# Optimization experiments

Measured on AMD Instinct MI355X. Metric: run time of the kernel, lower is better.

## Reference

```python
import jax, jax.numpy as jnp
import numpy as np

N = 100000
E = 1600000
CIN = 32
COUT = 32
K = 5
EPS = 1e-15      # PyG GMMConv EPS in sigma^2 denominator
BN_EPS = 1e-5    # torch BatchNorm1d default eps


def gmm_conv(x, edge_index, edge_attr, g, mu, sigma, root, bias):
    """PyG GMMConv (MoNet), aggr='mean', root_weight=True, bias=True."""
    src, dst = edge_index[0], edge_index[1]
    n = x.shape[0]
    k = mu.shape[0]
    cout = root.shape[1]
    xg = (x @ g).reshape(n, k, cout)                # [N, K, out]
    xj = xg[src]                                    # gather: [E, K, out]
    d = edge_attr[:, None, :] - mu[None, :, :]      # [E, K, 3]
    w = jnp.exp(-0.5 * jnp.sum(d * d / (EPS + sigma[None] ** 2), axis=-1))  # [E, K]
    msg = jnp.einsum('eko,ek->eo', xj, w)           # [E, out]
    agg = jax.ops.segment_sum(msg, dst, num_segments=n)
    cnt = jax.ops.segment_sum(jnp.ones((msg.shape[0],), x.dtype), dst, num_segments=n)
    agg = agg / jnp.clip(cnt, 1.0)[:, None]         # mean aggregation
    return agg + x @ root + bias


def batch_norm(x, gamma, beta):
    # training-mode BatchNorm1d: biased batch statistics over node dim
    m = x.mean(0)
    v = x.var(0)
    return (x - m) * jax.lax.rsqrt(v + BN_EPS) * gamma + beta


def setup_inputs() -> dict:
    key = jax.random.key(0)
    ks = jax.random.split(key, 12)
    p = lambda k, s, sc=0.1: jax.random.normal(k, s, jnp.float32) * sc
    return {
        'x': jax.random.normal(ks[0], (N, CIN), jnp.float32),
        'edge_index': jax.random.randint(ks[1], (2, E), 0, N, jnp.int32),
        'edge_attr': jax.random.uniform(ks[2], (E, 3), jnp.float32),
        # left conv1: in -> out, K=5
        'g1': p(ks[3], (CIN, K * COUT)), 'mu1': p(ks[4], (K, 3), 1.0), 'sigma1': jnp.ones((K, 3), jnp.float32),
        'root1': p(ks[5], (CIN, COUT)), 'b1': jnp.zeros((COUT,), jnp.float32),
        'gam1': jnp.ones((COUT,), jnp.float32), 'bet1': jnp.zeros((COUT,), jnp.float32),
        # left conv2: out -> out, K=5
        'g2': p(ks[6], (COUT, K * COUT)), 'mu2': p(ks[7], (K, 3), 1.0), 'sigma2': jnp.ones((K, 3), jnp.float32),
        'root2': p(ks[8], (COUT, COUT)), 'b2': jnp.zeros((COUT,), jnp.float32),
        'gam2': jnp.ones((COUT,), jnp.float32), 'bet2': jnp.zeros((COUT,), jnp.float32),
        # shortcut conv: in -> out, K=1
        'gs': p(ks[9], (CIN, 1 * COUT)), 'mus': p(ks[10], (1, 3), 1.0), 'sigmas': jnp.ones((1, 3), jnp.float32),
        'roots': p(ks[11], (CIN, COUT)), 'bs': jnp.zeros((COUT,), jnp.float32),
        'gams': jnp.ones((COUT,), jnp.float32), 'bets': jnp.zeros((COUT,), jnp.float32),
    }


def reference(x, edge_index, edge_attr,
              g1, mu1, sigma1, root1, b1, gam1, bet1,
              g2, mu2, sigma2, root2, b2, gam2, bet2,
              gs, mus, sigmas, roots, bs, gams, bets):
    h = jax.nn.elu(batch_norm(gmm_conv(x, edge_index, edge_attr, g1, mu1, sigma1, root1, b1), gam1, bet1))
    h = batch_norm(gmm_conv(h, edge_index, edge_attr, g2, mu2, sigma2, root2, b2), gam2, bet2)
    s = batch_norm(gmm_conv(x, edge_index, edge_attr, gs, mus, sigmas, roots, bs), gams, bets)
    return jax.nn.elu(h + s)
```

## Files before the change

### kernel.cpp

```cpp
#include <hip/hip_runtime.h>
#include <hip/hip_bf16.h>
#include <math.h>


#define ELU(v) ((v) > 0.f ? (v) : (__expf(v) - 1.f))

using short8  = __attribute__((ext_vector_type(8))) short;
using floatx4 = __attribute__((ext_vector_type(4))) float;

__device__ inline ushort f2bf(float f) {
    __hip_bfloat16 h = __float2bfloat16(f);
    return *reinterpret_cast<ushort*>(&h);
}
__device__ inline float bflo(unsigned u) { return __uint_as_float(u << 16); }
__device__ inline float bfhi(unsigned u) { return __uint_as_float(u & 0xffff0000u); }
__device__ inline unsigned pack_bf2(float lo, float hi) {
    return ((unsigned)f2bf(hi) << 16) | (unsigned)f2bf(lo);
}

__global__ __launch_bounds__(256) void prep_xb(
    const float* __restrict__ x, unsigned* __restrict__ XB, int N)
{
    const int idx = blockIdx.x * blockDim.x + threadIdx.x;
    if (idx >= N * 16) return;
    const float2 p = ((const float2*)x)[idx];
    XB[idx] = pack_bf2(p.x, p.y);
}

__global__ __launch_bounds__(256) void prep_hxb(
    const float* __restrict__ out1, const float* __restrict__ coef,
    unsigned* __restrict__ XB, int N)
{
    const int idx = blockIdx.x * blockDim.x + threadIdx.x;
    if (idx >= N * 16) return;
    const int l = idx & 15;
    const float2 p = ((const float2*)out1)[idx];
    const int c0 = 2 * l, c1 = 2 * l + 1;
    float v0 = p.x * coef[c0] + coef[32 + c0];
    float v1 = p.y * coef[c1] + coef[32 + c1];
    v0 = ELU(v0); v1 = ELU(v1);
    XB[idx] = pack_bf2(v0, v1);
}

#define CH 4096
__global__ __launch_bounds__(256) void binfill_k(
    const int* __restrict__ ei, const float* __restrict__ attr,
    int* __restrict__ gcur, unsigned long long* __restrict__ pay0,
    int E, int NB, int CAPc)
{
    __shared__ unsigned long long srec[CH];
    __shared__ unsigned char sbin[CH];
    __shared__ int cnt[256], offs[256], wcur[256], gbase[256], sc[256];

    const int t = threadIdx.x;
    const int e0 = blockIdx.x * CH;
    const int nrec = min(CH, E - e0);

    cnt[t] = 0;
    __syncthreads();

    unsigned long long rec[16];
    int bin[16];
#pragma unroll
    for (int r = 0; r < 16; ++r) {
        const int e = e0 + r * 256 + t;
        bin[r] = -1;
        if (e < E) {
            const int s = ei[e], d = ei[E + e];
            const float a0 = attr[(size_t)e * 3 + 0];
            const float a1 = attr[(size_t)e * 3 + 1];
            const float a2 = attr[(size_t)e * 3 + 2];
            const unsigned q0 = (unsigned)min(max((int)(a0 * 4096.f), 0), 4095);
            const unsigned q1 = (unsigned)min(max((int)(a1 * 4096.f), 0), 4095);
            const unsigned q2 = (unsigned)min(max((int)(a2 * 4096.f), 0), 4095);
            rec[r] = (unsigned long long)(unsigned)s
                   | ((unsigned long long)(d & 511) << 17)
                   | ((unsigned long long)q0 << 26)
                   | ((unsigned long long)q1 << 38)
                   | ((unsigned long long)q2 << 50);
            bin[r] = d >> 9;
            atomicAdd(&cnt[bin[r]], 1);
        }
    }
    __syncthreads();

    const int v = cnt[t];
    sc[t] = v;
    __syncthreads();
    for (int o = 1; o < 256; o <<= 1) {
        const int xx = (t >= o) ? sc[t - o] : 0;
        __syncthreads();
        sc[t] += xx;
        __syncthreads();
    }
    offs[t] = sc[t] - v;
    wcur[t] = sc[t] - v;
    __syncthreads();

#pragma unroll
    for (int r = 0; r < 16; ++r) {
        if (bin[r] >= 0) {
            const int pos = atomicAdd(&wcur[bin[r]], 1);
            srec[pos] = rec[r];
            sbin[pos] = (unsigned char)bin[r];
        }
    }
    __syncthreads();

    if (t < NB && cnt[t] > 0) gbase[t] = atomicAdd(&gcur[t], cnt[t]);
    __syncthreads();

    for (int i = t; i < nrec; i += 256) {
        const int b = sbin[i];
        const int idx = gbase[b] + (i - offs[b]);
        if (idx < CAPc)
            pay0[(size_t)b * CAPc + idx] = srec[i];
    }
}

__global__ __launch_bounds__(256) void scatter2_k(
    const unsigned long long* __restrict__ pay0, const int* __restrict__ gcur,
    int* __restrict__ row_ptr, unsigned long long* __restrict__ pay,
    int N, int CAPc, int NB)
{
    const int b = blockIdx.x;
    const int t = threadIdx.x;
    const int d0 = b << 9;
    const int nd = min(512, N - d0);

    __shared__ int cnt[512];
    __shared__ int offs[512];
    __shared__ int sscan[256];
    __shared__ int ssum[256];

    ssum[t] = (t < b && t < NB) ? gcur[t] : 0;
    for (int i = t; i < 512; i += 256) cnt[i] = 0;
    __syncthreads();
    for (int o = 128; o > 0; o >>= 1) {
        if (t < o) ssum[t] += ssum[t + o];
        __syncthreads();
    }
    const int base = ssum[0];

    const int total = min(gcur[b], CAPc);
    const unsigned long long* src = pay0 + (size_t)b * CAPc;

    for (int i = t; i < total; i += 256) {
        const int dlo = (int)((src[i] >> 17) & 511);
        atomicAdd(&cnt[dlo], 1);
    }
    __syncthreads();

    const int c0 = cnt[2 * t], c1 = cnt[2 * t + 1];
    const int pairsum = c0 + c1;
    sscan[t] = pairsum;
    __syncthreads();
    for (int o = 1; o < 256; o <<= 1) {
        const int xx = (t >= o) ? sscan[t - o] : 0;
        __syncthreads();
        sscan[t] += xx;
        __syncthreads();
    }
    const int excl = sscan[t] - pairsum;
    offs[2 * t] = excl;
    offs[2 * t + 1] = excl + c0;
    __syncthreads();
    const int btotal = sscan[255];

    for (int i = t; i < nd; i += 256) row_ptr[d0 + i] = base + offs[i];
    if (b == NB - 1 && t == 0) row_ptr[N] = base + btotal;

    for (int i = t; i < 512; i += 256) cnt[i] = offs[i];
    __syncthreads();

    for (int i = t; i < total; i += 256) {
        const unsigned long long rec = src[i];
        const int dlo = (int)((rec >> 17) & 511);
        const int p = atomicAdd(&cnt[dlo], 1);
        pay[base + p] = rec;
    }
}

template <bool HAS_S>
__global__ __launch_bounds__(256) void gt_k(
    const unsigned* __restrict__ XB,
    const unsigned long long* __restrict__ payload,
    const int* __restrict__ row_ptr,
    const float* __restrict__ mu_m, const float* __restrict__ sg_m,
    const float* __restrict__ mu_s, const float* __restrict__ sg_s,
    const float* __restrict__ g,
    const float* __restrict__ rootm,
    const float* __restrict__ bm,
    const float* __restrict__ gss,
    const float* __restrict__ rootss,
    const float* __restrict__ bss,
    float* __restrict__ out_m, float* __restrict__ out_s,
    float* __restrict__ stats_m, float* __restrict__ stats_s,
    int N, int ntiles)
{
    constexpr int KS = HAS_S ? 6 : 5;
    constexpr int SLS = KS + 1;
    constexpr int STRIDE = SLS * 16 + 4;
    constexpr float DQ = 1.0f / 4096.0f;

    __shared__ float wbuf[16][17][8];
    __shared__ unsigned sA[16 * STRIDE];
    __shared__ float sred[128];

    const int tid = threadIdx.x;
    const int l = tid & 15, grp = tid >> 4;
    const int lane = tid & 63, l4 = lane & 15, quad = lane >> 4;
    const int wv = tid >> 6;
    const int half = wv & 1;

    const bool convRole = (wv < 2);
    const bool sRole = HAS_S && (wv >= 2);
    short8 Bf[6];
    float bias0 = 0.f;
    if (convRole) {
#pragma unroll
        for (int s = 0; s < 5; ++s)
#pragma unroll
            for (int j = 0; j < 8; ++j)
                Bf[s][j] = (short)f2bf(g[(quad * 8 + j) * 160 + s * 32 + 16 * half + l4]);
#pragma unroll
        for (int j = 0; j < 8; ++j)
            Bf[5][j] = (short)f2bf(rootm[(quad * 8 + j) * 32 + 16 * half + l4]);
        bias0 = bm[16 * half + l4];
    } else if (sRole) {
#pragma unroll
        for (int j = 0; j < 8; ++j) {
            Bf[0][j] = (short)f2bf(gss[(quad * 8 + j) * 32 + 16 * half + l4]);
            Bf[1][j] = (short)f2bf(rootss[(quad * 8 + j) * 32 + 16 * half + l4]);
        }
        bias0 = bss[16 * half + l4];
    }

    float mm[15], im[15];
#pragma unroll
    for (int i = 0; i < 15; ++i) {
        mm[i] = mu_m[i];
        float s = sg_m[i];
        im[i] = 1.0f / (1e-15f + s * s);
    }
    float ms[3], is[3];
    if (HAS_S) {
#pragma unroll
        for (int i = 0; i < 3; ++i) {
            ms[i] = mu_s[i];
            float s = sg_s[i];
            is[i] = 1.0f / (1e-15f + s * s);
        }
    }

    float ps = 0.f, pq = 0.f;

    for (int tile = blockIdx.x; tile < ntiles; tile += gridDim.x) {
        const int dst = tile * 16 + grp;
        float2 acc[KS];
#pragma unroll
        for (int k = 0; k < KS; ++k) acc[k] = make_float2(0.f, 0.f);

        int rp0 = 0, deg = 0;
        if (dst < N) { rp0 = row_ptr[dst]; deg = row_ptr[dst + 1] - rp0; }

        auto body = [&](int j) {
            const float4 a = *(const float4*)&wbuf[grp][j][0];
            const float4 b = *(const float4*)&wbuf[grp][j][4];
            const int sj = __float_as_int(a.x);
            const unsigned u = XB[(size_t)sj * 16 + l];
            const float x0 = bflo(u), x1 = bfhi(u);
            acc[0].x = fmaf(a.y, x0, acc[0].x); acc[0].y = fmaf(a.y, x1, acc[0].y);
            acc[1].x = fmaf(a.z, x0, acc[1].x); acc[1].y = fmaf(a.z, x1, acc[1].y);
            acc[2].x = fmaf(a.w, x0, acc[2].x); acc[2].y = fmaf(a.w, x1, acc[2].y);
            acc[3].x = fmaf(b.x, x0, acc[3].x); acc[3].y = fmaf(b.x, x1, acc[3].y);
            acc[4].x = fmaf(b.y, x0, acc[4].x); acc[4].y = fmaf(b.y, x1, acc[4].y);
            if (HAS_S) {
                acc[5].x = fmaf(b.z, x0, acc[5].x); acc[5].y = fmaf(b.z, x1, acc[5].y);
            }
        };

        for (int base = 0; base < deg; base += 16) {
            const int nj = min(16, deg - base);
            if (l < nj) {
                unsigned long long pq8 = payload[rp0 + base + l];
                const int src = (int)(pq8 & 0x1FFFFull);
                float p0 = ((int)((pq8 >> 26) & 0xFFF) + 0.5f) * DQ;
                float p1 = ((int)((pq8 >> 38) & 0xFFF) + 0.5f) * DQ;
                float p2 = ((int)((pq8 >> 50) & 0xFFF) + 0.5f) * DQ;
                float w[5], wS = 0.f;
#pragma unroll
                for (int k = 0; k < 5; ++k) {
                    float d0 = p0 - mm[k * 3 + 0];
                    float d1 = p1 - mm[k * 3 + 1];
                    float d2 = p2 - mm[k * 3 + 2];
                    float q = d0 * d0 * im[k * 3 + 0] + d1 * d1 * im[k * 3 + 1]
                            + d2 * d2 * im[k * 3 + 2];
                    w[k] = __expf(-0.5f * q);
                }
                if (HAS_S) {
                    float d0 = p0 - ms[0], d1 = p1 - ms[1], d2 = p2 - ms[2];
                    float q = d0 * d0 * is[0] + d1 * d1 * is[1] + d2 * d2 * is[2];
                    wS = __expf(-0.5f * q);
                }
                float4* wp = (float4*)&wbuf[grp][l][0];
                wp[0] = make_float4(__int_as_float(src), w[0], w[1], w[2]);
                wp[1] = make_float4(w[3], w[4], wS, 0.f);
            }
            int j = 0;
            for (; j + 3 < nj; j += 4) { body(j); body(j + 1); body(j + 2); body(j + 3); }
            for (; j < nj; ++j) body(j);
        }

        {
            unsigned* arow = sA + grp * STRIDE;
            const float invd = 1.0f / fmaxf((float)deg, 1.0f);
            const bool ok = (dst < N);
#pragma unroll
            for (int k = 0; k < KS; ++k)
                arow[k * 16 + l] = ok ? pack_bf2(acc[k].x * invd, acc[k].y * invd) : 0u;
            arow[KS * 16 + l] = ok ? XB[(size_t)dst * 16 + l] : 0u;
        }
        __syncthreads();

        if (convRole || sRole) {
            floatx4 C = {0.f, 0.f, 0.f, 0.f};
            if (convRole) {
#pragma unroll
                for (int s = 0; s < 6; ++s) {
                    const int slot = (s < 5) ? s : KS;
                    const uint4 av = *(const uint4*)(sA + l4 * STRIDE + slot * 16 + quad * 4);
                    const short8 A = *reinterpret_cast<const short8*>(&av);
                    C = __builtin_amdgcn_mfma_f32_16x16x32_bf16(A, Bf[s], C, 0, 0, 0);
                }
            } else {
#pragma unroll
                for (int s = 0; s < 2; ++s) {
                    const int slot = 5 + s;
                    const uint4 av = *(const uint4*)(sA + l4 * STRIDE + slot * 16 + quad * 4);
                    const short8 A = *reinterpret_cast<const short8*>(&av);
                    C = __builtin_amdgcn_mfma_f32_16x16x32_bf16(A, Bf[s], C, 0, 0, 0);
                }
            }

            float* outp = convRole ? out_m : out_s;
#pragma unroll
            for (int r = 0; r < 4; ++r) {
                const int n = tile * 16 + quad * 4 + r;
                if (n < N) {
                    const float v = C[r] + bias0;
                    outp[(size_t)n * 32 + 16 * half + l4] = v;
                    ps += v; pq += v * v;
                }
            }
        }
        __syncthreads();
    }

    if (tid < 128) sred[tid] = 0.f;
    __syncthreads();
    if (convRole) {
        atomicAdd(&sred[16 * half + l4], ps);
        atomicAdd(&sred[32 + 16 * half + l4], pq);
    } else if (sRole) {
        atomicAdd(&sred[64 + 16 * half + l4], ps);
        atomicAdd(&sred[96 + 16 * half + l4], pq);
    }
    __syncthreads();
    const int spread = (blockIdx.x & 7) * 64;
    if (tid < 64) atomicAdd(&stats_m[spread + tid], sred[tid]);
    else if (HAS_S && tid < 128) atomicAdd(&stats_s[spread + tid - 64], sred[tid]);
}

__global__ void coef2_k(const float* __restrict__ stats1, const float* __restrict__ gam1,
                        const float* __restrict__ bet1, float* __restrict__ coef1,
                        const float* __restrict__ stats2, const float* __restrict__ gam2,
                        const float* __restrict__ bet2, float* __restrict__ coef2,
                        float invN)
{
    const int t = threadIdx.x;
    const int set = t >> 6;
    const int c = t & 63;
    if (c >= 32) return;
    const float* stats = set ? stats2 : stats1;
    const float* gam = set ? gam2 : gam1;
    const float* bet = set ? bet2 : bet1;
    float* coef = set ? coef2 : coef1;
    if (set && !stats) return;
    float s = 0.f, q = 0.f;
    for (int p = 0; p < 8; ++p) { s += stats[p * 64 + c]; q += stats[p * 64 + 32 + c]; }
    float m = s * invN;
    float v = fmaxf(q * invN - m * m, 0.f);
    float sc = gam[c] * rsqrtf(v + 1e-5f);
    coef[c] = sc;
    coef[32 + c] = bet[c] - m * sc;
}

__global__ __launch_bounds__(256) void final_k(
    const float* __restrict__ o2, const float* __restrict__ os,
    const float* __restrict__ c2, const float* __restrict__ cs,
    float* __restrict__ out, int total)
{
    int idx = blockIdx.x * blockDim.x + threadIdx.x;
    if (idx >= total) return;
    int c = idx & 31;
    float v = o2[idx] * c2[c] + c2[32 + c] + os[idx] * cs[c] + cs[32 + c];
    out[idx] = ELU(v);
}

extern "C" void kernel_launch(void* const* d_in, const int* in_sizes, int n_in,
                              void* d_out, int out_size, void* d_ws, size_t ws_size,
                              hipStream_t stream)
{
    const float* x      = (const float*)d_in[0];
    const int*   ei     = (const int*)d_in[1];
    const float* attr   = (const float*)d_in[2];
    const float* g1     = (const float*)d_in[3];
    const float* mu1    = (const float*)d_in[4];
    const float* sig1   = (const float*)d_in[5];
    const float* root1  = (const float*)d_in[6];
    const float* b1     = (const float*)d_in[7];
    const float* gam1   = (const float*)d_in[8];
    const float* bet1   = (const float*)d_in[9];
    const float* g2     = (const float*)d_in[10];
    const float* mu2    = (const float*)d_in[11];
    const float* sig2   = (const float*)d_in[12];
    const float* root2  = (const float*)d_in[13];
    const float* b2     = (const float*)d_in[14];
    const float* gam2   = (const float*)d_in[15];
    const float* bet2   = (const float*)d_in[16];
    const float* gs     = (const float*)d_in[17];
    const float* mus    = (const float*)d_in[18];
    const float* sigs   = (const float*)d_in[19];
    const float* roots  = (const float*)d_in[20];
    const float* bs     = (const float*)d_in[21];
    const float* gams   = (const float*)d_in[22];
    const float* bets   = (const float*)d_in[23];

    const int N = in_sizes[0] / 32;
    const int E = in_sizes[1] / 2;
    const int total = N * 32;
    const int ntiles = (N + 15) / 16;
    const int NB = (N + 511) >> 9;
    const int CAPc = ((((E + NB - 1) / NB) * 5) / 4 + 15) & ~15;

    char* ws = (char*)d_ws;
    size_t off = 0;
    auto carve = [&](size_t bytes) {
        void* p = ws + off;
        off = (off + bytes + 255) & ~(size_t)255;
        return p;
    };
    unsigned* XB   = (unsigned*)carve((size_t)N * 16 * 4);
    float*  OUT1   = (float*)carve((size_t)N * 32 * 4);
    float*  OUT2   = (float*)carve((size_t)N * 32 * 4);
    float*  OUTS   = (float*)carve((size_t)N * 32 * 4);
    unsigned long long* PAY  = (unsigned long long*)carve((size_t)E * 8);
    unsigned long long* PAY0 = (unsigned long long*)carve((size_t)NB * CAPc * 8);
    int*    ROWP   = (int*)carve((size_t)(N + 1) * 4);
    int*    GCUR   = (int*)carve(256 * 4);
    float*  STATS  = (float*)carve(3 * 512 * 4);
    float*  COEF   = (float*)carve(3 * 64 * 4);
    float* stats1 = STATS, *stats2 = STATS + 512, *statsS = STATS + 1024;
    float* coef1 = COEF, *coef2 = COEF + 64, *coefS = COEF + 128;
    (void)ws_size; (void)n_in; (void)out_size;

    const float invN = 1.0f / (float)N;
    const int ew = (total + 255) / 256;
    const int epb = (N * 16 + 255) / 256;
    const int nfb = (E + CH - 1) / CH;
    const int gtb = ntiles < 2048 ? ntiles : 2048;

    hipMemsetAsync(GCUR, 0, 256 * 4, stream);
    hipMemsetAsync(STATS, 0, 3 * 512 * 4, stream);

    binfill_k<<<nfb, 256, 0, stream>>>(ei, attr, GCUR, PAY0, E, NB, CAPc);
    scatter2_k<<<NB, 256, 0, stream>>>(PAY0, GCUR, ROWP, PAY, N, CAPc, NB);

    prep_xb<<<epb, 256, 0, stream>>>(x, XB, N);
    gt_k<true><<<gtb, 256, 0, stream>>>(XB, PAY, ROWP,
        mu1, sig1, mus, sigs, g1, root1, b1, gs, roots, bs,
        OUT1, OUTS, stats1, statsS, N, ntiles);
    coef2_k<<<1, 128, 0, stream>>>(stats1, gam1, bet1, coef1,
                                   statsS, gams, bets, coefS, invN);

    prep_hxb<<<epb, 256, 0, stream>>>(OUT1, coef1, XB, N);
    gt_k<false><<<gtb, 256, 0, stream>>>(XB, PAY, ROWP,
        mu2, sig2, nullptr, nullptr, g2, root2, b2, nullptr, nullptr, nullptr,
        OUT2, nullptr, stats2, nullptr, N, ntiles);
    coef2_k<<<1, 128, 0, stream>>>(stats2, gam2, bet2, coef2,
                                   nullptr, nullptr, nullptr, nullptr, invN);

    final_k<<<ew, 256, 0, stream>>>(OUT2, OUTS, coef2, coefS, (float*)d_out, total);
}
```

Measured before the change: 324.2 us.

## Double-buffer MFMA staging, fold x conversion into binfill, merge memsets

The gather-tile kernel now double-buffers its shared A tile and runs the MFMA and output stage for the previous tile after staging the current one. This removes one block-wide barrier per tile and lets matrix work overlap the gather. The standalone x-to-bf16 conversion kernel is folded into the binning kernel, and the two memsets are merged into one, which relies on GCUR and STATS sitting next to each other in the workspace. The grid cap drops from 2048 to 1536 blocks, and shared memory grows for the second buffer.

```diff
diff --git a/kernel.cpp b/kernel.cpp
--- a/kernel.cpp
+++ b/kernel.cpp
@@ -16,15 +16,6 @@
 __device__ inline float bfhi(unsigned u) { return __uint_as_float(u & 0xffff0000u); }
 __device__ inline unsigned pack_bf2(float lo, float hi) {
     return ((unsigned)f2bf(hi) << 16) | (unsigned)f2bf(lo);
-}
-
-__global__ __launch_bounds__(256) void prep_xb(
-    const float* __restrict__ x, unsigned* __restrict__ XB, int N)
-{
-    const int idx = blockIdx.x * blockDim.x + threadIdx.x;
-    if (idx >= N * 16) return;
-    const float2 p = ((const float2*)x)[idx];
-    XB[idx] = pack_bf2(p.x, p.y);
 }
 
 __global__ __launch_bounds__(256) void prep_hxb(
@@ -46,6 +37,7 @@
 __global__ __launch_bounds__(256) void binfill_k(
     const int* __restrict__ ei, const float* __restrict__ attr,
     int* __restrict__ gcur, unsigned long long* __restrict__ pay0,
+    const float* __restrict__ x, unsigned* __restrict__ XB, int nxb,
     int E, int NB, int CAPc)
 {
     __shared__ unsigned long long srec[CH];
@@ -55,6 +47,14 @@
     const int t = threadIdx.x;
     const int e0 = blockIdx.x * CH;
     const int nrec = min(CH, E - e0);
+
+    for (int i = t; i < CH; i += 256) {
+        const int idx = e0 + i;
+        if (idx < nxb) {
+            const float2 p = ((const float2*)x)[idx];
+            XB[idx] = pack_bf2(p.x, p.y);
+        }
+    }
 
     cnt[t] = 0;
     __syncthreads();
@@ -204,7 +204,7 @@
     constexpr float DQ = 1.0f / 4096.0f;
 
     __shared__ float wbuf[16][17][8];
-    __shared__ unsigned sA[16 * STRIDE];
+    __shared__ unsigned sA[2][16 * STRIDE];
     __shared__ float sred[128];
 
     const int tid = threadIdx.x;
@@ -254,6 +254,41 @@
     }
 
     float ps = 0.f, pq = 0.f;
+
+    auto mfma_tile = [&](int b, int tileDone) {
+        if (!(convRole || sRole)) return;
+        const unsigned* sAb = sA[b];
+        floatx4 C = {0.f, 0.f, 0.f, 0.f};
+        if (convRole) {
+#pragma unroll
+            for (int s = 0; s < 6; ++s) {
+                const int slot = (s < 5) ? s : KS;
+                const uint4 av = *(const uint4*)(sAb + l4 * STRIDE + slot * 16 + quad * 4);
+                const short8 A = *reinterpret_cast<const short8*>(&av);
+                C = __builtin_amdgcn_mfma_f32_16x16x32_bf16(A, Bf[s], C, 0, 0, 0);
+            }
+        } else {
+#pragma unroll
+            for (int s = 0; s < 2; ++s) {
+                const int slot = 5 + s;
+                const uint4 av = *(const uint4*)(sAb + l4 * STRIDE + slot * 16 + quad * 4);
+                const short8 A = *reinterpret_cast<const short8*>(&av);
+                C = __builtin_amdgcn_mfma_f32_16x16x32_bf16(A, Bf[s], C, 0, 0, 0);
+            }
+        }
+        float* outp = convRole ? out_m : out_s;
+#pragma unroll
+        for (int r = 0; r < 4; ++r) {
+            const int n = tileDone * 16 + quad * 4 + r;
+            if (n < N) {
+                const float v = C[r] + bias0;
+                outp[(size_t)n * 32 + 16 * half + l4] = v;
+                ps += v; pq += v * v;
+            }
+        }
+    };
+
+    int p = 0, prevTile = -1;
 
     for (int tile = blockIdx.x; tile < ntiles; tile += gridDim.x) {
         const int dst = tile * 16 + grp;
@@ -313,7 +348,7 @@
         }
 
         {
-            unsigned* arow = sA + grp * STRIDE;
+            unsigned* arow = sA[p] + grp * STRIDE;
             const float invd = 1.0f / fmaxf((float)deg, 1.0f);
             const bool ok = (dst < N);
 #pragma unroll
@@ -321,41 +356,14 @@
                 arow[k * 16 + l] = ok ? pack_bf2(acc[k].x * invd, acc[k].y * invd) : 0u;
             arow[KS * 16 + l] = ok ? XB[(size_t)dst * 16 + l] : 0u;
         }
+
+        if (prevTile >= 0) mfma_tile(1 - p, prevTile);
+
         __syncthreads();
-
-        if (convRole || sRole) {
-            floatx4 C = {0.f, 0.f, 0.f, 0.f};
-            if (convRole) {
-#pragma unroll
-                for (int s = 0; s < 6; ++s) {
-                    const int slot = (s < 5) ? s : KS;
-                    const uint4 av = *(const uint4*)(sA + l4 * STRIDE + slot * 16 + quad * 4);
-                    const short8 A = *reinterpret_cast<const short8*>(&av);
-                    C = __builtin_amdgcn_mfma_f32_16x16x32_bf16(A, Bf[s], C, 0, 0, 0);
-                }
-            } else {
-#pragma unroll
-                for (int s = 0; s < 2; ++s) {
-                    const int slot = 5 + s;
-                    const uint4 av = *(const uint4*)(sA + l4 * STRIDE + slot * 16 + quad * 4);
-                    const short8 A = *reinterpret_cast<const short8*>(&av);
-                    C = __builtin_amdgcn_mfma_f32_16x16x32_bf16(A, Bf[s], C, 0, 0, 0);
-                }
-            }
-
-            float* outp = convRole ? out_m : out_s;
-#pragma unroll
-            for (int r = 0; r < 4; ++r) {
-                const int n = tile * 16 + quad * 4 + r;
-                if (n < N) {
-                    const float v = C[r] + bias0;
-                    outp[(size_t)n * 32 + 16 * half + l4] = v;
-                    ps += v; pq += v * v;
-                }
-            }
-        }
-        __syncthreads();
-    }
+        prevTile = tile;
+        p ^= 1;
+    }
+    if (prevTile >= 0) mfma_tile(1 - p, prevTile);
 
     if (tid < 128) sred[tid] = 0.f;
     __syncthreads();
@@ -469,15 +477,13 @@
     const int ew = (total + 255) / 256;
     const int epb = (N * 16 + 255) / 256;
     const int nfb = (E + CH - 1) / CH;
-    const int gtb = ntiles < 2048 ? ntiles : 2048;
-
-    hipMemsetAsync(GCUR, 0, 256 * 4, stream);
-    hipMemsetAsync(STATS, 0, 3 * 512 * 4, stream);
-
-    binfill_k<<<nfb, 256, 0, stream>>>(ei, attr, GCUR, PAY0, E, NB, CAPc);
+    const int gtb = ntiles < 1536 ? ntiles : 1536;
+
+    hipMemsetAsync(GCUR, 0, 256 * 4 + 3 * 512 * 4, stream);
+
+    binfill_k<<<nfb, 256, 0, stream>>>(ei, attr, GCUR, PAY0, x, XB, N * 16, E, NB, CAPc);
     scatter2_k<<<NB, 256, 0, stream>>>(PAY0, GCUR, ROWP, PAY, N, CAPc, NB);
 
-    prep_xb<<<epb, 256, 0, stream>>>(x, XB, N);
     gt_k<true><<<gtb, 256, 0, stream>>>(XB, PAY, ROWP,
         mu1, sig1, mus, sigs, g1, root1, b1, gs, roots, bs,
         OUT1, OUTS, stats1, statsS, N, ntiles);
```

Result: no change. 327.7 us (+1.1%).
